# Performance work log

Measured on AMD Instinct MI355X. Metric: run time of the kernel, lower is better.

## Reference

```python
import jax, jax.numpy as jnp
import numpy as np

B, S, H, N_ITEMS = 1024, 200, 256, 50000


def setup_inputs() -> dict:
    key = jax.random.key(0)
    ks = jax.random.split(key, 10)
    s = 0.05
    x = jax.random.randint(ks[0], (B, S), 0, N_ITEMS)
    # timestamps: increasing along the sequence
    t = jnp.sort(jax.random.uniform(ks[1], (B, S), dtype=jnp.float32) * 10.0, axis=1)
    item_emb = (jax.random.normal(ks[2], (N_ITEMS, H), dtype=jnp.float32) * s).at[0].set(0.0)  # padding_idx=0
    W_ih = jax.random.normal(ks[3], (3 * H, H), dtype=jnp.float32) * s
    W_hh = jax.random.normal(ks[4], (3 * H, H), dtype=jnp.float32) * s
    b_ih = jnp.zeros((3 * H,), jnp.float32)
    b_hh = jnp.zeros((3 * H,), jnp.float32)
    W1 = jax.random.normal(ks[5], (H, H), dtype=jnp.float32) * s
    b1 = jnp.zeros((H,), jnp.float32)
    W2 = jax.random.normal(ks[6], (H, H), dtype=jnp.float32) * s
    b2 = jnp.zeros((H,), jnp.float32)
    W_head = jax.random.normal(ks[7], (N_ITEMS, H), dtype=jnp.float32) * s
    b_head = jnp.zeros((N_ITEMS,), jnp.float32)
    return dict(x=x, t=t, item_emb=item_emb, W_ih=W_ih, W_hh=W_hh, b_ih=b_ih,
                b_hh=b_hh, W1=W1, b1=b1, W2=W2, b2=b2, W_head=W_head, b_head=b_head)


def _gru_cell(xe, h, W_ih, W_hh, b_ih, b_hh):
    # PyTorch GRUCell: gates ordered (r, z, n)
    gi = xe @ W_ih.T + b_ih  # [B, 3H]
    gh = h @ W_hh.T + b_hh
    i_r, i_z, i_n = jnp.split(gi, 3, axis=-1)
    h_r, h_z, h_n = jnp.split(gh, 3, axis=-1)
    r = jax.nn.sigmoid(i_r + h_r)
    z = jax.nn.sigmoid(i_z + h_z)
    n = jnp.tanh(i_n + r * h_n)
    return (1.0 - z) * n + z * h


def _ode_f(h, W1, b1, W2, b2):
    # ODEFunc: MLP on hidden state (t-independent)
    return jnp.tanh(h @ W1.T + b1) @ W2.T + b2


def _rk4_step(h, dt, W1, b1, W2, b2):
    # dt: [B, 1]; dt == 0 on the last step => identity (matches i < seq_len-1 guard)
    f = lambda hh: _ode_f(hh, W1, b1, W2, b2)
    k1 = f(h)
    k2 = f(h + 0.5 * dt * k1)
    k3 = f(h + 0.5 * dt * k2)
    k4 = f(h + dt * k3)
    return h + (dt / 6.0) * (k1 + 2.0 * k2 + 2.0 * k3 + k4)


def reference(x, t, item_emb, W_ih, W_hh, b_ih, b_hh, W1, b1, W2, b2, W_head, b_head):
    x_emb = item_emb[x]  # [B, S, H]
    bsz = x.shape[0]
    # dt_i = max(t_{i+1}, t_i + 1e-5) - t_i for i < S-1, 0 for the final step
    t_next = jnp.maximum(t[:, 1:], t[:, :-1] + 1e-5)
    dt = jnp.concatenate([t_next - t[:, :-1], jnp.zeros((bsz, 1), t.dtype)], axis=1)  # [B, S]
    xs = (jnp.swapaxes(x_emb, 0, 1), jnp.swapaxes(dt, 0, 1)[..., None])  # [S,B,H], [S,B,1]
    h0 = jnp.zeros((bsz, x_emb.shape[-1]), x_emb.dtype)

    def step(h, inp):
        xe, dts = inp
        h = _gru_cell(xe, h, W_ih, W_hh, b_ih, b_hh)
        h = _rk4_step(h, dts, W1, b1, W2, b2)
        return h, None

    h, _ = jax.lax.scan(step, h0, xs)
    return h @ W_head.T + b_head  # [B, n_items]
```

## Files before the change

kernel.cpp:

```cpp
#include <hip/hip_runtime.h>


#define B_SZ   1024
#define S_LEN  200
#define HD     256
#define NITEMS 50000
#define NPAD   50048

#define OFF_WHH 0
#define OFF_WIH 196608
#define OFF_W1  393216
#define OFF_W2  458752
#define OFF_BHH 524288
#define OFF_BIH 525056
#define OFF_B1  525824
#define OFF_B2  526080
#define CANON_N 526336

typedef short short8 __attribute__((ext_vector_type(8)));
typedef float f32x4  __attribute__((ext_vector_type(4)));

__device__ __forceinline__ float bf2f(unsigned short u){
  unsigned v = ((unsigned)u) << 16; float f; __builtin_memcpy(&f, &v, 4); return f;
}
__device__ __forceinline__ unsigned short f2bf(float f){
  unsigned u; __builtin_memcpy(&u, &f, 4);
  u += 0x7FFFu + ((u >> 16) & 1u);
  return (unsigned short)(u >> 16);
}
__device__ __forceinline__ float fsig(float x){ return 1.0f / (1.0f + __expf(-x)); }
__device__ __forceinline__ float ftanh(float x){
  float e = __expf(-2.0f * fabsf(x));
  float r = (1.0f - e) / (1.0f + e);
  return copysignf(r, x);
}
__device__ __forceinline__ f32x4 MFMA(short8 a, short8 b, f32x4 c){
  return __builtin_amdgcn_mfma_f32_16x16x32_bf16(a, b, c, 0, 0, 0);
}
__device__ __forceinline__ int foff(int kc, int row){
  return (kc * 16 + ((row ^ kc) & 15)) * 8;
}

__global__ void sniff_kernel(const unsigned short* __restrict__ t, int* __restrict__ flag){
  int lane = threadIdx.x & 63;
  int bad = 0;
#pragma unroll
  for (int q = 0; q < 8; ++q)
    if (t[lane * 8 + q] > 0x4200u) bad = 1;
  unsigned long long m = __ballot(bad);
  if (lane == 0) flag[0] = (m != 0ull) ? 1 : 0;
}

__global__ void conv_kernel(const int* __restrict__ flag,
    const void* __restrict__ Whh, const void* __restrict__ Wih,
    const void* __restrict__ W1,  const void* __restrict__ W2,
    const void* __restrict__ bhh, const void* __restrict__ bih,
    const void* __restrict__ b1,  const void* __restrict__ b2,
    unsigned short* __restrict__ dst)
{
  int i = blockIdx.x * 256 + threadIdx.x;
  if (i >= CANON_N) return;
  int f32m = flag[0];
  const void* src; int off = i;
  if (i < OFF_WIH)      { src = Whh; off = i - OFF_WHH; }
  else if (i < OFF_W1)  { src = Wih; off = i - OFF_WIH; }
  else if (i < OFF_W2)  { src = W1;  off = i - OFF_W1; }
  else if (i < OFF_BHH) { src = W2;  off = i - OFF_W2; }
  else if (i < OFF_BIH) { src = bhh; off = i - OFF_BHH; }
  else if (i < OFF_B1)  { src = bih; off = i - OFF_BIH; }
  else if (i < OFF_B2)  { src = b1;  off = i - OFF_B1; }
  else                  { src = b2;  off = i - OFF_B2; }
  unsigned short v = f32m ? f2bf(((const float*)src)[off])
                          : ((const unsigned short*)src)[off];
  dst[i] = v;
}

__global__ void convw_kernel(const int* __restrict__ flag,
    const void* __restrict__ Wh, unsigned short* __restrict__ dst)
{
  int i4 = blockIdx.x * 256 + threadIdx.x;
  if (i4 * 4 >= NITEMS * HD) return;
  if (flag[0]){
    f32x4 v = ((const f32x4*)Wh)[i4];
#pragma unroll
    for (int q = 0; q < 4; ++q) dst[i4 * 4 + q] = f2bf(v[q]);
  } else {
    ((unsigned long long*)dst)[i4] = ((const unsigned long long*)Wh)[i4];
  }
}

__global__ void dt_kernel(const void* __restrict__ t, const int* __restrict__ flag,
                          float* __restrict__ dt){
  int i = blockIdx.x * 256 + threadIdx.x;
  if (i >= B_SZ * S_LEN) return;
  int f32m = flag[0];
  int s = i % S_LEN;
  float tc = f32m ? ((const float*)t)[i] : bf2f(((const unsigned short*)t)[i]);
  float d = 0.0f;
  if (s < S_LEN - 1){
    float tn = f32m ? ((const float*)t)[i + 1] : bf2f(((const unsigned short*)t)[i + 1]);
    d = fmaxf(tn, tc + 1e-5f) - tc;
  }
  dt[i] = d;
}

__global__ __launch_bounds__(256) void gitems_kernel(
    const void* __restrict__ emb, const unsigned short* __restrict__ canon,
    const int* __restrict__ flag, void* __restrict__ tbl, int tblf32)
{
  __shared__ __align__(16) short ap[4][4096];
  const int tid = threadIdx.x;
  const int i0 = blockIdx.x * 64;
  const int n0 = blockIdx.y * 256;
  const int f32m = flag[0];
  {
    int kc = tid & 31, r8 = tid >> 5;
#pragma unroll
    for (int p = 0; p < 8; ++p){
      int row = p * 8 + r8;
      int gr = i0 + row; if (gr > NITEMS - 1) gr = NITEMS - 1;
      short8 v;
      if (f32m){
        const f32x4* src = (const f32x4*)((const float*)emb + gr * HD + kc * 8);
        f32x4 v0 = src[0], v1 = src[1];
#pragma unroll
        for (int q = 0; q < 4; ++q){ v[q] = (short)f2bf(v0[q]); v[4+q] = (short)f2bf(v1[q]); }
      } else {
        v = *(const short8*)((const unsigned short*)emb + gr * HD + kc * 8);
      }
      *(short8*)&ap[row >> 4][foff(kc, row & 15)] = v;
    }
  }
  __syncthreads();
  const int wave = tid >> 6, lane = tid & 63, col = lane & 15, quad = lane >> 4;
  const unsigned short* Wih = canon + OFF_WIH;
  const unsigned short* bih = canon + OFF_BIH;
  f32x4 zz = {0.0f, 0.0f, 0.0f, 0.0f};
  f32x4 acc[4][4];
#pragma unroll
  for (int rt = 0; rt < 4; ++rt)
#pragma unroll
    for (int ct = 0; ct < 4; ++ct) acc[rt][ct] = zz;

#pragma unroll
  for (int ks = 0; ks < 8; ++ks){
    short8 bf[4];
#pragma unroll
    for (int ct = 0; ct < 4; ++ct){
      int n = n0 + wave * 64 + ct * 16 + col;
      bf[ct] = *(const short8*)(Wih + n * HD + ks * 32 + quad * 8);
    }
    int kc = ks * 4 + quad;
#pragma unroll
    for (int rt = 0; rt < 4; ++rt){
      short8 a = *(const short8*)&ap[rt][foff(kc, col)];
#pragma unroll
      for (int ct = 0; ct < 4; ++ct) acc[rt][ct] = MFMA(a, bf[ct], acc[rt][ct]);
    }
  }
  float bv[4];
#pragma unroll
  for (int ct = 0; ct < 4; ++ct) bv[ct] = bf2f(bih[n0 + wave * 64 + ct * 16 + col]);
  float* tfo = (float*)tbl; unsigned short* tbo = (unsigned short*)tbl;
#pragma unroll
  for (int rt = 0; rt < 4; ++rt)
#pragma unroll
    for (int ct = 0; ct < 4; ++ct)
#pragma unroll
      for (int r = 0; r < 4; ++r){
        int row = i0 + rt * 16 + quad * 4 + r;
        if (row < NITEMS){
          int n = n0 + wave * 64 + ct * 16 + col;
          float v = acc[rt][ct][r] + bv[ct];
          if (tblf32) tfo[row * 768 + n] = v;
          else        tbo[row * 768 + n] = (unsigned short)f2bf(v);
        }
      }
}

__global__ __launch_bounds__(512, 2) void scan_kernel(
    const int* __restrict__ x, const float* __restrict__ dtp,
    const unsigned short* __restrict__ canon,
    const void* __restrict__ tbl, int tblf32,
    float* __restrict__ hstate)
{
  __shared__ __align__(16) short bufhi[2][4096];
  __shared__ __align__(16) short buflo[2][4096];
  __shared__ float dtl[16];

  const int tid  = threadIdx.x;
  const int wave = tid >> 6;
  const int lane = tid & 63;
  const int col  = lane & 15;
  const int quad = lane >> 4;
  const int r0   = blockIdx.x * 16;
  const int wc0  = wave * 32;

  const unsigned short* Whh = canon + OFF_WHH;
  const unsigned short* W1w = canon + OFF_W1;
  const unsigned short* W2w = canon + OFF_W2;
  const unsigned short* bhh = canon + OFF_BHH;
  const unsigned short* b1v = canon + OFF_B1;
  const unsigned short* b2v = canon + OFF_B2;

  {
    short8 z = {0,0,0,0,0,0,0,0};
    *(short8*)&bufhi[0][tid * 8] = z;
    *(short8*)&buflo[0][tid * 8] = z;
  }

  short8 w1f[2][8], w2f[2][8];
#pragma unroll
  for (int ct = 0; ct < 2; ++ct){
    int n = wc0 + ct * 16 + col;
#pragma unroll
    for (int ks = 0; ks < 8; ++ks){
      w1f[ct][ks] = *(const short8*)(W1w + n * HD + ks * 32 + quad * 8);
      w2f[ct][ks] = *(const short8*)(W2w + n * HD + ks * 32 + quad * 8);
    }
  }
  float bR[2], bZ[2], bN[2], b1c[2], b2c[2];
#pragma unroll
  for (int ct = 0; ct < 2; ++ct){
    int c = wc0 + ct * 16 + col;
    bR[ct]  = bf2f(bhh[c]);          bZ[ct] = bf2f(bhh[HD + c]);
    bN[ct]  = bf2f(bhh[2 * HD + c]);
    b1c[ct] = bf2f(b1v[c]);          b2c[ct] = bf2f(b2v[c]);
  }

  float h[2][4];
#pragma unroll
  for (int ct = 0; ct < 2; ++ct)
#pragma unroll
    for (int r = 0; r < 4; ++r) h[ct][r] = 0.0f;

  const float* tf = (const float*)tbl;
  const unsigned short* tb = (const unsigned short*)tbl;

  __syncthreads();

  for (int s = 0; s < S_LEN; ++s){
    const int pb = s & 1;
    if (tid < 16) dtl[tid] = dtp[(r0 + tid) * S_LEN + s];

    f32x4 aR[2], aZ[2], aN[2];
    float giN[2][4];
#pragma unroll
    for (int r = 0; r < 4; ++r){
      int row = quad * 4 + r;
      int it = x[(r0 + row) * S_LEN + s];
      long base = (long)it * 768;
#pragma unroll
      for (int ct = 0; ct < 2; ++ct){
        int c = wc0 + ct * 16 + col;
        float gr, gz, gn;
        if (tblf32){ gr = tf[base + c]; gz = tf[base + 256 + c]; gn = tf[base + 512 + c]; }
        else { gr = bf2f(tb[base + c]); gz = bf2f(tb[base + 256 + c]); gn = bf2f(tb[base + 512 + c]); }
        aR[ct][r] = gr; aZ[ct][r] = gz; aN[ct][r] = 0.0f; giN[ct][r] = gn;
      }
    }
#pragma unroll
    for (int ks = 0; ks < 8; ++ks){
      int kc = ks * 4 + quad;
      short8 ahi = *(const short8*)&bufhi[pb][foff(kc, col)];
      short8 alo = *(const short8*)&buflo[pb][foff(kc, col)];
#pragma unroll
      for (int ct = 0; ct < 2; ++ct){
        int nb = wc0 + ct * 16 + col;
        short8 b0 = *(const short8*)(Whh + (0 * HD + nb) * HD + ks * 32 + quad * 8);
        aR[ct] = MFMA(ahi, b0, aR[ct]); aR[ct] = MFMA(alo, b0, aR[ct]);
        short8 b1f = *(const short8*)(Whh + (1 * HD + nb) * HD + ks * 32 + quad * 8);
        aZ[ct] = MFMA(ahi, b1f, aZ[ct]); aZ[ct] = MFMA(alo, b1f, aZ[ct]);
        short8 b2f = *(const short8*)(Whh + (2 * HD + nb) * HD + ks * 32 + quad * 8);
        aN[ct] = MFMA(ahi, b2f, aN[ct]); aN[ct] = MFMA(alo, b2f, aN[ct]);
      }
    }
    float hg[2][4], ksum[2][4];
#pragma unroll
    for (int ct = 0; ct < 2; ++ct)
#pragma unroll
      for (int r = 0; r < 4; ++r){
        int row = quad * 4 + r;
        float rr = fsig(aR[ct][r] + bR[ct]);
        float z_ = fsig(aZ[ct][r] + bZ[ct]);
        float nn = ftanh(giN[ct][r] + rr * (aN[ct][r] + bN[ct]));
        float hgv = (1.0f - z_) * nn + z_ * h[ct][r];
        hg[ct][r] = hgv;
        int c = wc0 + ct * 16 + col;
        bufhi[1 - pb][foff(c >> 3, row) + (c & 7)] = (short)f2bf(hgv);
      }
    __syncthreads();

#pragma unroll
    for (int j = 0; j < 4; ++j){
      f32x4 ua[2];
      ua[0] = (f32x4){b1c[0], b1c[0], b1c[0], b1c[0]};
      ua[1] = (f32x4){b1c[1], b1c[1], b1c[1], b1c[1]};
#pragma unroll
      for (int ks = 0; ks < 8; ++ks){
        int kc = ks * 4 + quad;
        short8 a = *(const short8*)&bufhi[1 - pb][foff(kc, col)];
        ua[0] = MFMA(a, w1f[0][ks], ua[0]);
        ua[1] = MFMA(a, w1f[1][ks], ua[1]);
      }
#pragma unroll
      for (int ct = 0; ct < 2; ++ct)
#pragma unroll
        for (int r = 0; r < 4; ++r){
          int row = quad * 4 + r, c = wc0 + ct * 16 + col;
          bufhi[pb][foff(c >> 3, row) + (c & 7)] = (short)f2bf(ftanh(ua[ct][r]));
        }
      __syncthreads();

      f32x4 ka[2];
      ka[0] = (f32x4){b2c[0], b2c[0], b2c[0], b2c[0]};
      ka[1] = (f32x4){b2c[1], b2c[1], b2c[1], b2c[1]};
#pragma unroll
      for (int ks = 0; ks < 8; ++ks){
        int kc = ks * 4 + quad;
        short8 a = *(const short8*)&bufhi[pb][foff(kc, col)];
        ka[0] = MFMA(a, w2f[0][ks], ka[0]);
        ka[1] = MFMA(a, w2f[1][ks], ka[1]);
      }
#pragma unroll
      for (int ct = 0; ct < 2; ++ct)
#pragma unroll
        for (int r = 0; r < 4; ++r){
          int row = quad * 4 + r;
          float dtv = dtl[row];
          float kv = ka[ct][r];
          int c = wc0 + ct * 16 + col;
          if (j == 0){
            ksum[ct][r] = kv;
            float y = hg[ct][r] + 0.5f * dtv * kv;
            bufhi[1 - pb][foff(c >> 3, row) + (c & 7)] = (short)f2bf(y);
          } else if (j == 1){
            ksum[ct][r] += 2.0f * kv;
            float y = hg[ct][r] + 0.5f * dtv * kv;
            bufhi[1 - pb][foff(c >> 3, row) + (c & 7)] = (short)f2bf(y);
          } else if (j == 2){
            ksum[ct][r] += 2.0f * kv;
            float y = hg[ct][r] + dtv * kv;
            bufhi[1 - pb][foff(c >> 3, row) + (c & 7)] = (short)f2bf(y);
          } else {
            ksum[ct][r] += kv;
            float hn = hg[ct][r] + (dtv * (1.0f / 6.0f)) * ksum[ct][r];
            h[ct][r] = hn;
            unsigned short hh = f2bf(hn);
            float fh = bf2f(hh);
            unsigned short hl = f2bf(hn - fh);
            bufhi[1 - pb][foff(c >> 3, row) + (c & 7)] = (short)hh;
            buflo[1 - pb][foff(c >> 3, row) + (c & 7)] = (short)hl;
          }
        }
      __syncthreads();
    }
  }
#pragma unroll
  for (int ct = 0; ct < 2; ++ct)
#pragma unroll
    for (int r = 0; r < 4; ++r){
      int row = quad * 4 + r;
      hstate[(r0 + row) * HD + wc0 + ct * 16 + col] = h[ct][r];
    }
}

__global__ __launch_bounds__(256) void head_kernel(
    const float* __restrict__ hstate,
    const unsigned short* __restrict__ Whb,
    const void* __restrict__ Wh,
    const void* __restrict__ bh, const int* __restrict__ flag, int wbf,
    void* __restrict__ outv)
{
  __shared__ __align__(16) short ahi[4][4096];
  __shared__ __align__(16) short alo[4][4096];
  const int tid = threadIdx.x;
  const int i0 = blockIdx.x * 64;
  const int n0 = blockIdx.y * 256;
  const int f32m = flag[0];
  {
    int kc = tid & 31, r8 = tid >> 5;
#pragma unroll
    for (int p = 0; p < 8; ++p){
      int row = p * 8 + r8;
      const float* src = hstate + (i0 + row) * HD + kc * 8;
      short8 vh, vl;
#pragma unroll
      for (int q = 0; q < 8; ++q){
        float f = src[q];
        unsigned short hb = f2bf(f);
        float fh = bf2f(hb);
        vh[q] = (short)hb; vl[q] = (short)f2bf(f - fh);
      }
      int off = foff(kc, row & 15);
      *(short8*)&ahi[row >> 4][off] = vh;
      *(short8*)&alo[row >> 4][off] = vl;
    }
  }
  __syncthreads();
  const int wave = tid >> 6, lane = tid & 63, col = lane & 15, quad = lane >> 4;
  f32x4 zz = {0.0f, 0.0f, 0.0f, 0.0f};
  f32x4 acc[4][4];
#pragma unroll
  for (int rt = 0; rt < 4; ++rt)
#pragma unroll
    for (int ct = 0; ct < 4; ++ct) acc[rt][ct] = zz;

  int nidx[4];
#pragma unroll
  for (int ct = 0; ct < 4; ++ct){
    int n = n0 + wave * 64 + ct * 16 + col;
    nidx[ct] = (n < NITEMS) ? n : (NITEMS - 1);
  }
#pragma unroll
  for (int ks = 0; ks < 8; ++ks){
    short8 bf[4];
#pragma unroll
    for (int ct = 0; ct < 4; ++ct){
      if (wbf){
        bf[ct] = *(const short8*)(Whb + nidx[ct] * HD + ks * 32 + quad * 8);
      } else if (f32m){
        const f32x4* src = (const f32x4*)((const float*)Wh + nidx[ct] * HD + ks * 32 + quad * 8);
        f32x4 v0 = src[0], v1 = src[1];
        short8 v;
#pragma unroll
        for (int q = 0; q < 4; ++q){ v[q] = (short)f2bf(v0[q]); v[4+q] = (short)f2bf(v1[q]); }
        bf[ct] = v;
      } else {
        bf[ct] = *(const short8*)((const unsigned short*)Wh + nidx[ct] * HD + ks * 32 + quad * 8);
      }
    }
    int kc = ks * 4 + quad;
#pragma unroll
    for (int rt = 0; rt < 4; ++rt){
      short8 xh = *(const short8*)&ahi[rt][foff(kc, col)];
      short8 xl = *(const short8*)&alo[rt][foff(kc, col)];
#pragma unroll
      for (int ct = 0; ct < 4; ++ct){
        acc[rt][ct] = MFMA(xh, bf[ct], acc[rt][ct]);
        acc[rt][ct] = MFMA(xl, bf[ct], acc[rt][ct]);
      }
    }
  }
  float bhv[4];
#pragma unroll
  for (int ct = 0; ct < 4; ++ct)
    bhv[ct] = f32m ? ((const float*)bh)[nidx[ct]] : bf2f(((const unsigned short*)bh)[nidx[ct]]);
  float* outf = (float*)outv;
  unsigned short* outb = (unsigned short*)outv;
#pragma unroll
  for (int rt = 0; rt < 4; ++rt)
#pragma unroll
    for (int ct = 0; ct < 4; ++ct)
#pragma unroll
      for (int r = 0; r < 4; ++r){
        int row = i0 + rt * 16 + quad * 4 + r;
        int n = n0 + wave * 64 + ct * 16 + col;
        if (n < NITEMS){
          float v = acc[rt][ct][r] + bhv[ct];
          long o = (long)row * NITEMS + n;
          if (f32m) outf[o] = v;
          else      outb[o] = (unsigned short)f2bf(v);
        }
      }
}

extern "C" void kernel_launch(void* const* d_in, const int* in_sizes, int n_in,
                              void* d_out, int out_size, void* d_ws, size_t ws_size,
                              hipStream_t stream) {
  const int*  x     = (const int*)d_in[0];
  const void* t     = d_in[1];
  const void* emb   = d_in[2];
  const void* Wih   = d_in[3];
  const void* Whh   = d_in[4];
  const void* bih   = d_in[5];
  const void* bhh   = d_in[6];
  const void* W1    = d_in[7];
  const void* b1    = d_in[8];
  const void* W2    = d_in[9];
  const void* b2    = d_in[10];
  const void* Whead = d_in[11];
  const void* bhead = d_in[12];

  char* ws = (char*)d_ws;
  int*   flag   = (int*)(ws);
  float* dtbuf  = (float*)(ws + 4096);
  float* hstate = (float*)(ws + (1u << 20));
  unsigned short* canon = (unsigned short*)(ws + (2u << 20));
  unsigned short* wheadb = (unsigned short*)(ws + (4u << 20));
  const size_t tbase = 32u << 20;
  const size_t TBL_F32  = (size_t)NPAD * 768 * 4;
  const size_t TBL_BF16 = (size_t)NPAD * 768 * 2;

  int wbf = (ws_size >= (32u << 20)) ? 1 : 0;
  void* tbl; int tblf32;
  if (ws_size >= tbase + TBL_F32)       { tbl = (void*)(ws + tbase); tblf32 = 1; }
  else if (ws_size >= tbase + TBL_BF16) { tbl = (void*)(ws + tbase); tblf32 = 0; }
  else                                  { tbl = (void*)d_out;        tblf32 = 0; }

  sniff_kernel<<<dim3(1), dim3(64), 0, stream>>>((const unsigned short*)t, flag);
  conv_kernel<<<dim3((CANON_N + 255) / 256), dim3(256), 0, stream>>>(
      flag, Whh, Wih, W1, W2, bhh, bih, b1, b2, canon);
  if (wbf)
    convw_kernel<<<dim3((NITEMS * HD / 4 + 255) / 256), dim3(256), 0, stream>>>(
        flag, Whead, wheadb);
  dt_kernel<<<dim3((B_SZ * S_LEN + 255) / 256), dim3(256), 0, stream>>>(t, flag, dtbuf);
  gitems_kernel<<<dim3(NPAD / 64, 3), dim3(256), 0, stream>>>(emb, canon, flag, tbl, tblf32);
  scan_kernel<<<dim3(64), dim3(512), 0, stream>>>(x, dtbuf, canon, tbl, tblf32, hstate);
  head_kernel<<<dim3(B_SZ / 64, (NITEMS + 255) / 256), dim3(256), 0, stream>>>(
      hstate, wheadb, Whead, bhead, flag, wbf, d_out);
}
```

Before: 5.033 ms.

## Prefetch next-step input-gate rows and stage token ids and dt in LDS

```diff
diff --git a/kernel.cpp b/kernel.cpp
--- a/kernel.cpp
+++ b/kernel.cpp
@@ -178,7 +178,8 @@
       }
 }
 
-__global__ __launch_bounds__(512, 2) void scan_kernel(
+__global__ __launch_bounds__(512) __attribute__((amdgpu_waves_per_eu(2, 2)))
+void scan_kernel(
     const int* __restrict__ x, const float* __restrict__ dtp,
     const unsigned short* __restrict__ canon,
     const void* __restrict__ tbl, int tblf32,
@@ -186,7 +187,8 @@
 {
   __shared__ __align__(16) short bufhi[2][4096];
   __shared__ __align__(16) short buflo[2][4096];
-  __shared__ float dtl[16];
+  __shared__ __align__(16) int   xl[16 * S_LEN];
+  __shared__ __align__(16) float dtall[16 * S_LEN];
 
   const int tid  = threadIdx.x;
   const int wave = tid >> 6;
@@ -208,6 +210,10 @@
     *(short8*)&bufhi[0][tid * 8] = z;
     *(short8*)&buflo[0][tid * 8] = z;
   }
+  for (int i = tid; i < 16 * S_LEN; i += 512){
+    xl[i]    = x[r0 * S_LEN + i];
+    dtall[i] = dtp[r0 * S_LEN + i];
+  }
 
   short8 w1f[2][8], w2f[2][8];
 #pragma unroll
@@ -239,26 +245,64 @@
 
   __syncthreads();
 
+  float gR[2][4], gZ[2][4], gN[2][4];
+#pragma unroll
+  for (int r = 0; r < 4; ++r){
+    long base = (long)xl[(quad * 4 + r) * S_LEN] * 768;
+#pragma unroll
+    for (int ct = 0; ct < 2; ++ct){
+      int c = wc0 + ct * 16 + col;
+      if (tblf32){
+        gR[ct][r] = __builtin_nontemporal_load(tf + base + c);
+        gZ[ct][r] = __builtin_nontemporal_load(tf + base + 256 + c);
+        gN[ct][r] = __builtin_nontemporal_load(tf + base + 512 + c);
+      } else {
+        gR[ct][r] = bf2f(__builtin_nontemporal_load(tb + base + c));
+        gZ[ct][r] = bf2f(__builtin_nontemporal_load(tb + base + 256 + c));
+        gN[ct][r] = bf2f(__builtin_nontemporal_load(tb + base + 512 + c));
+      }
+    }
+  }
+
   for (int s = 0; s < S_LEN; ++s){
     const int pb = s & 1;
-    if (tid < 16) dtl[tid] = dtp[(r0 + tid) * S_LEN + s];
+    float dtr[4];
+#pragma unroll
+    for (int r = 0; r < 4; ++r) dtr[r] = dtall[(quad * 4 + r) * S_LEN + s];
 
     f32x4 aR[2], aZ[2], aN[2];
     float giN[2][4];
 #pragma unroll
-    for (int r = 0; r < 4; ++r){
-      int row = quad * 4 + r;
-      int it = x[(r0 + row) * S_LEN + s];
-      long base = (long)it * 768;
-#pragma unroll
-      for (int ct = 0; ct < 2; ++ct){
-        int c = wc0 + ct * 16 + col;
-        float gr, gz, gn;
-        if (tblf32){ gr = tf[base + c]; gz = tf[base + 256 + c]; gn = tf[base + 512 + c]; }
-        else { gr = bf2f(tb[base + c]); gz = bf2f(tb[base + 256 + c]); gn = bf2f(tb[base + 512 + c]); }
-        aR[ct][r] = gr; aZ[ct][r] = gz; aN[ct][r] = 0.0f; giN[ct][r] = gn;
-      }
-    }
+    for (int ct = 0; ct < 2; ++ct)
+#pragma unroll
+      for (int r = 0; r < 4; ++r){
+        aR[ct][r] = gR[ct][r];
+        aZ[ct][r] = gZ[ct][r];
+        aN[ct][r] = 0.0f;
+        giN[ct][r] = gN[ct][r];
+      }
+
+    {
+      int sn = (s + 1 < S_LEN) ? s + 1 : S_LEN - 1;
+#pragma unroll
+      for (int r = 0; r < 4; ++r){
+        long base = (long)xl[(quad * 4 + r) * S_LEN + sn] * 768;
+#pragma unroll
+        for (int ct = 0; ct < 2; ++ct){
+          int c = wc0 + ct * 16 + col;
+          if (tblf32){
+            gR[ct][r] = __builtin_nontemporal_load(tf + base + c);
+            gZ[ct][r] = __builtin_nontemporal_load(tf + base + 256 + c);
+            gN[ct][r] = __builtin_nontemporal_load(tf + base + 512 + c);
+          } else {
+            gR[ct][r] = bf2f(__builtin_nontemporal_load(tb + base + c));
+            gZ[ct][r] = bf2f(__builtin_nontemporal_load(tb + base + 256 + c));
+            gN[ct][r] = bf2f(__builtin_nontemporal_load(tb + base + 512 + c));
+          }
+        }
+      }
+    }
+
 #pragma unroll
     for (int ks = 0; ks < 8; ++ks){
       int kc = ks * 4 + quad;
@@ -327,7 +371,7 @@
 #pragma unroll
         for (int r = 0; r < 4; ++r){
           int row = quad * 4 + r;
-          float dtv = dtl[row];
+          float dtv = dtr[r];
           float kv = ka[ct][r];
           int c = wc0 + ct * 16 + col;
           if (j == 0){
```

Result: slower. 5.473 ms (+8.7%).

## Stream ODE weights from global, preload token ids and dt into LDS

Applied to the files above, without the earlier changes.

```diff
diff --git a/kernel.cpp b/kernel.cpp
--- a/kernel.cpp
+++ b/kernel.cpp
@@ -178,7 +178,8 @@
       }
 }
 
-__global__ __launch_bounds__(512, 2) void scan_kernel(
+__global__ __launch_bounds__(512)
+void scan_kernel(
     const int* __restrict__ x, const float* __restrict__ dtp,
     const unsigned short* __restrict__ canon,
     const void* __restrict__ tbl, int tblf32,
@@ -186,7 +187,8 @@
 {
   __shared__ __align__(16) short bufhi[2][4096];
   __shared__ __align__(16) short buflo[2][4096];
-  __shared__ float dtl[16];
+  __shared__ __align__(16) int   xl[16 * S_LEN];
+  __shared__ __align__(16) float dtall[16 * S_LEN];
 
   const int tid  = threadIdx.x;
   const int wave = tid >> 6;
@@ -208,17 +210,11 @@
     *(short8*)&bufhi[0][tid * 8] = z;
     *(short8*)&buflo[0][tid * 8] = z;
   }
-
-  short8 w1f[2][8], w2f[2][8];
-#pragma unroll
-  for (int ct = 0; ct < 2; ++ct){
-    int n = wc0 + ct * 16 + col;
-#pragma unroll
-    for (int ks = 0; ks < 8; ++ks){
-      w1f[ct][ks] = *(const short8*)(W1w + n * HD + ks * 32 + quad * 8);
-      w2f[ct][ks] = *(const short8*)(W2w + n * HD + ks * 32 + quad * 8);
-    }
-  }
+  for (int i = tid; i < 16 * S_LEN; i += 512){
+    xl[i]    = x[r0 * S_LEN + i];
+    dtall[i] = dtp[r0 * S_LEN + i];
+  }
+
   float bR[2], bZ[2], bN[2], b1c[2], b2c[2];
 #pragma unroll
   for (int ct = 0; ct < 2; ++ct){
@@ -241,21 +237,29 @@
 
   for (int s = 0; s < S_LEN; ++s){
     const int pb = s & 1;
-    if (tid < 16) dtl[tid] = dtp[(r0 + tid) * S_LEN + s];
+    float dtr[4];
+#pragma unroll
+    for (int r = 0; r < 4; ++r) dtr[r] = dtall[(quad * 4 + r) * S_LEN + s];
 
     f32x4 aR[2], aZ[2], aN[2];
     float giN[2][4];
 #pragma unroll
     for (int r = 0; r < 4; ++r){
       int row = quad * 4 + r;
-      int it = x[(r0 + row) * S_LEN + s];
-      long base = (long)it * 768;
+      long base = (long)xl[row * S_LEN + s] * 768;
 #pragma unroll
       for (int ct = 0; ct < 2; ++ct){
         int c = wc0 + ct * 16 + col;
         float gr, gz, gn;
-        if (tblf32){ gr = tf[base + c]; gz = tf[base + 256 + c]; gn = tf[base + 512 + c]; }
-        else { gr = bf2f(tb[base + c]); gz = bf2f(tb[base + 256 + c]); gn = bf2f(tb[base + 512 + c]); }
+        if (tblf32){
+          gr = __builtin_nontemporal_load(tf + base + c);
+          gz = __builtin_nontemporal_load(tf + base + 256 + c);
+          gn = __builtin_nontemporal_load(tf + base + 512 + c);
+        } else {
+          gr = bf2f(__builtin_nontemporal_load(tb + base + c));
+          gz = bf2f(__builtin_nontemporal_load(tb + base + 256 + c));
+          gn = bf2f(__builtin_nontemporal_load(tb + base + 512 + c));
+        }
         aR[ct][r] = gr; aZ[ct][r] = gz; aN[ct][r] = 0.0f; giN[ct][r] = gn;
       }
     }
@@ -300,8 +304,11 @@
       for (int ks = 0; ks < 8; ++ks){
         int kc = ks * 4 + quad;
         short8 a = *(const short8*)&bufhi[1 - pb][foff(kc, col)];
-        ua[0] = MFMA(a, w1f[0][ks], ua[0]);
-        ua[1] = MFMA(a, w1f[1][ks], ua[1]);
+#pragma unroll
+        for (int ct = 0; ct < 2; ++ct){
+          short8 w = *(const short8*)(W1w + (wc0 + ct * 16 + col) * HD + ks * 32 + quad * 8);
+          ua[ct] = MFMA(a, w, ua[ct]);
+        }
       }
 #pragma unroll
       for (int ct = 0; ct < 2; ++ct)
@@ -319,15 +326,18 @@
       for (int ks = 0; ks < 8; ++ks){
         int kc = ks * 4 + quad;
         short8 a = *(const short8*)&bufhi[pb][foff(kc, col)];
-        ka[0] = MFMA(a, w2f[0][ks], ka[0]);
-        ka[1] = MFMA(a, w2f[1][ks], ka[1]);
+#pragma unroll
+        for (int ct = 0; ct < 2; ++ct){
+          short8 w = *(const short8*)(W2w + (wc0 + ct * 16 + col) * HD + ks * 32 + quad * 8);
+          ka[ct] = MFMA(a, w, ka[ct]);
+        }
       }
 #pragma unroll
       for (int ct = 0; ct < 2; ++ct)
 #pragma unroll
         for (int r = 0; r < 4; ++r){
           int row = quad * 4 + r;
-          float dtv = dtl[row];
+          float dtv = dtr[r];
           float kv = ka[ct][r];
           int c = wc0 + ct * 16 + col;
           if (j == 0){
```

Measured after the change: 4.580 ms. -9.0%, faster.

## Move W2 fragments to LDS, restructure GRU gate loop to batch Whh loads

Applied to the files above, without the earlier changes.

```diff
diff --git a/kernel.cpp b/kernel.cpp
--- a/kernel.cpp
+++ b/kernel.cpp
@@ -178,15 +178,16 @@
       }
 }
 
-__global__ __launch_bounds__(512, 2) void scan_kernel(
+__global__ __launch_bounds__(512)
+void scan_kernel(
     const int* __restrict__ x, const float* __restrict__ dtp,
     const unsigned short* __restrict__ canon,
     const void* __restrict__ tbl, int tblf32,
     float* __restrict__ hstate)
 {
   __shared__ __align__(16) short bufhi[2][4096];
-  __shared__ __align__(16) short buflo[2][4096];
-  __shared__ float dtl[16];
+  __shared__ __align__(16) short buflo[4096];
+  __shared__ __align__(16) short w2lds[16][4096];
 
   const int tid  = threadIdx.x;
   const int wave = tid >> 6;
@@ -203,21 +204,24 @@
   const unsigned short* b1v = canon + OFF_B1;
   const unsigned short* b2v = canon + OFF_B2;
 
+  for (int c = tid; c < 8192; c += 512){
+    int kc = c & 31, row = (c >> 5) & 15, t = c >> 9;
+    *(short8*)&w2lds[t][foff(kc, row)] =
+        *(const short8*)(W2w + (t * 16 + row) * HD + kc * 8);
+  }
   {
     short8 z = {0,0,0,0,0,0,0,0};
     *(short8*)&bufhi[0][tid * 8] = z;
-    *(short8*)&buflo[0][tid * 8] = z;
-  }
-
-  short8 w1f[2][8], w2f[2][8];
+    *(short8*)&buflo[tid * 8] = z;
+  }
+
+  short8 w1f[2][8];
 #pragma unroll
   for (int ct = 0; ct < 2; ++ct){
     int n = wc0 + ct * 16 + col;
 #pragma unroll
-    for (int ks = 0; ks < 8; ++ks){
+    for (int ks = 0; ks < 8; ++ks)
       w1f[ct][ks] = *(const short8*)(W1w + n * HD + ks * 32 + quad * 8);
-      w2f[ct][ks] = *(const short8*)(W2w + n * HD + ks * 32 + quad * 8);
-    }
   }
   float bR[2], bZ[2], bN[2], b1c[2], b2c[2];
 #pragma unroll
@@ -241,54 +245,65 @@
 
   for (int s = 0; s < S_LEN; ++s){
     const int pb = s & 1;
-    if (tid < 16) dtl[tid] = dtp[(r0 + tid) * S_LEN + s];
-
-    f32x4 aR[2], aZ[2], aN[2];
-    float giN[2][4];
+    int xi[4]; float dtr[4];
 #pragma unroll
     for (int r = 0; r < 4; ++r){
       int row = quad * 4 + r;
-      int it = x[(r0 + row) * S_LEN + s];
-      long base = (long)it * 768;
-#pragma unroll
-      for (int ct = 0; ct < 2; ++ct){
-        int c = wc0 + ct * 16 + col;
-        float gr, gz, gn;
-        if (tblf32){ gr = tf[base + c]; gz = tf[base + 256 + c]; gn = tf[base + 512 + c]; }
-        else { gr = bf2f(tb[base + c]); gz = bf2f(tb[base + 256 + c]); gn = bf2f(tb[base + 512 + c]); }
-        aR[ct][r] = gr; aZ[ct][r] = gz; aN[ct][r] = 0.0f; giN[ct][r] = gn;
-      }
-    }
-#pragma unroll
-    for (int ks = 0; ks < 8; ++ks){
-      int kc = ks * 4 + quad;
-      short8 ahi = *(const short8*)&bufhi[pb][foff(kc, col)];
-      short8 alo = *(const short8*)&buflo[pb][foff(kc, col)];
-#pragma unroll
-      for (int ct = 0; ct < 2; ++ct){
-        int nb = wc0 + ct * 16 + col;
-        short8 b0 = *(const short8*)(Whh + (0 * HD + nb) * HD + ks * 32 + quad * 8);
-        aR[ct] = MFMA(ahi, b0, aR[ct]); aR[ct] = MFMA(alo, b0, aR[ct]);
-        short8 b1f = *(const short8*)(Whh + (1 * HD + nb) * HD + ks * 32 + quad * 8);
-        aZ[ct] = MFMA(ahi, b1f, aZ[ct]); aZ[ct] = MFMA(alo, b1f, aZ[ct]);
-        short8 b2f = *(const short8*)(Whh + (2 * HD + nb) * HD + ks * 32 + quad * 8);
-        aN[ct] = MFMA(ahi, b2f, aN[ct]); aN[ct] = MFMA(alo, b2f, aN[ct]);
-      }
-    }
+      xi[r]  = x[(r0 + row) * S_LEN + s];
+      dtr[r] = dtp[(r0 + row) * S_LEN + s];
+    }
+
     float hg[2][4], ksum[2][4];
 #pragma unroll
-    for (int ct = 0; ct < 2; ++ct)
+    for (int ct = 0; ct < 2; ++ct){
+      const int nb = wc0 + ct * 16 + col;
+      f32x4 aR, aZ, aN;
+      float giN[4];
+#pragma unroll
+      for (int r = 0; r < 4; ++r){
+        long base = (long)xi[r] * 768;
+        if (tblf32){
+          aR[r]  = __builtin_nontemporal_load(tf + base + nb);
+          aZ[r]  = __builtin_nontemporal_load(tf + base + 256 + nb);
+          giN[r] = __builtin_nontemporal_load(tf + base + 512 + nb);
+        } else {
+          aR[r]  = bf2f(__builtin_nontemporal_load(tb + base + nb));
+          aZ[r]  = bf2f(__builtin_nontemporal_load(tb + base + 256 + nb));
+          giN[r] = bf2f(__builtin_nontemporal_load(tb + base + 512 + nb));
+        }
+        aN[r] = 0.0f;
+      }
+      short8 wb[8];
+#pragma unroll
+      for (int g = 0; g < 3; ++g){
+#pragma unroll
+        for (int ks = 0; ks < 8; ++ks)
+          wb[ks] = *(const short8*)(Whh + (g * HD + nb) * HD + ks * 32 + quad * 8);
+        __builtin_amdgcn_sched_barrier(0);
+        f32x4 acc = {0.0f, 0.0f, 0.0f, 0.0f};
+#pragma unroll
+        for (int ks = 0; ks < 8; ++ks){
+          int kc = ks * 4 + quad;
+          short8 ahi = *(const short8*)&bufhi[pb][foff(kc, col)];
+          short8 alo = *(const short8*)&buflo[foff(kc, col)];
+          acc = MFMA(ahi, wb[ks], acc);
+          acc = MFMA(alo, wb[ks], acc);
+        }
+        if (g == 0)      aR += acc;
+        else if (g == 1) aZ += acc;
+        else             aN += acc;
+      }
 #pragma unroll
       for (int r = 0; r < 4; ++r){
         int row = quad * 4 + r;
-        float rr = fsig(aR[ct][r] + bR[ct]);
-        float z_ = fsig(aZ[ct][r] + bZ[ct]);
-        float nn = ftanh(giN[ct][r] + rr * (aN[ct][r] + bN[ct]));
+        float rr = fsig(aR[r] + bR[ct]);
+        float z_ = fsig(aZ[r] + bZ[ct]);
+        float nn = ftanh(giN[r] + rr * (aN[r] + bN[ct]));
         float hgv = (1.0f - z_) * nn + z_ * h[ct][r];
         hg[ct][r] = hgv;
-        int c = wc0 + ct * 16 + col;
-        bufhi[1 - pb][foff(c >> 3, row) + (c & 7)] = (short)f2bf(hgv);
-      }
+        bufhi[1 - pb][foff(nb >> 3, row) + (nb & 7)] = (short)f2bf(hgv);
+      }
+    }
     __syncthreads();
 
 #pragma unroll
@@ -319,15 +334,17 @@
       for (int ks = 0; ks < 8; ++ks){
         int kc = ks * 4 + quad;
         short8 a = *(const short8*)&bufhi[pb][foff(kc, col)];
-        ka[0] = MFMA(a, w2f[0][ks], ka[0]);
-        ka[1] = MFMA(a, w2f[1][ks], ka[1]);
+        short8 w20 = *(const short8*)&w2lds[wave * 2 + 0][foff(kc, col)];
+        short8 w21 = *(const short8*)&w2lds[wave * 2 + 1][foff(kc, col)];
+        ka[0] = MFMA(a, w20, ka[0]);
+        ka[1] = MFMA(a, w21, ka[1]);
       }
 #pragma unroll
       for (int ct = 0; ct < 2; ++ct)
 #pragma unroll
         for (int r = 0; r < 4; ++r){
           int row = quad * 4 + r;
-          float dtv = dtl[row];
+          float dtv = dtr[r];
           float kv = ka[ct][r];
           int c = wc0 + ct * 16 + col;
           if (j == 0){
@@ -348,9 +365,8 @@
             h[ct][r] = hn;
             unsigned short hh = f2bf(hn);
             float fh = bf2f(hh);
-            unsigned short hl = f2bf(hn - fh);
             bufhi[1 - pb][foff(c >> 3, row) + (c & 7)] = (short)hh;
-            buflo[1 - pb][foff(c >> 3, row) + (c & 7)] = (short)hl;
+            buflo[foff(c >> 3, row) + (c & 7)] = (short)f2bf(hn - fh);
           }
         }
       __syncthreads();
@@ -434,11 +450,11 @@
 #pragma unroll
     for (int rt = 0; rt < 4; ++rt){
       short8 xh = *(const short8*)&ahi[rt][foff(kc, col)];
-      short8 xl = *(const short8*)&alo[rt][foff(kc, col)];
+      short8 xl2 = *(const short8*)&alo[rt][foff(kc, col)];
 #pragma unroll
       for (int ct = 0; ct < 4; ++ct){
         acc[rt][ct] = MFMA(xh, bf[ct], acc[rt][ct]);
-        acc[rt][ct] = MFMA(xl, bf[ct], acc[rt][ct]);
+        acc[rt][ct] = MFMA(xl2, bf[ct], acc[rt][ct]);
       }
     }
   }
```

After: 4.370 ms. -13.2%, faster.
